# Optimization experiments

Measured on AMD Instinct MI355X. Metric: run time of the kernel, lower is better.

Reference implementation:

```python
import jax, jax.numpy as jnp
import numpy as np

B, C, H, W = 4, 96, 256, 256
WS = 8          # window size
NH = 4          # num heads
SHIFT = 4       # shift size (block_idx=1 -> WS//2)
HD = C // NH    # head dim = 24
N = WS * WS     # tokens per window = 64
MLP_H = 4 * C   # 384
EPS = 1e-6


def _rel_pos_index():
    coords = np.stack(np.meshgrid(np.arange(WS), np.arange(WS), indexing='ij'))  # [2,WS,WS]
    cf = coords.reshape(2, -1)                                                   # [2,N]
    rel = cf[:, :, None] - cf[:, None, :]                                        # [2,N,N]
    rel = rel.transpose(1, 2, 0) + (WS - 1)
    rel[:, :, 0] *= 2 * WS - 1
    return rel.sum(-1)  # [N,N] int


def _attn_mask():
    # standard Swin shifted-window mask, static (numpy)
    img = np.zeros((H, W), dtype=np.float32)
    cnt = 0
    for hs in (slice(0, -WS), slice(-WS, -SHIFT), slice(-SHIFT, None)):
        for ws_ in (slice(0, -WS), slice(-WS, -SHIFT), slice(-SHIFT, None)):
            img[hs, ws_] = cnt
            cnt += 1
    m = img.reshape(H // WS, WS, W // WS, WS).transpose(0, 2, 1, 3).reshape(-1, N)  # [nW,N]
    am = m[:, None, :] - m[:, :, None]
    return np.where(am != 0, -100.0, 0.0).astype(np.float32)  # [nW,N,N]


REL_IDX = _rel_pos_index()
ATTN_MASK = _attn_mask()


def _ln(x, w, b):
    mu = x.mean(-1, keepdims=True)
    var = ((x - mu) ** 2).mean(-1, keepdims=True)
    return (x - mu) * jax.lax.rsqrt(var + EPS) * w + b


def setup_inputs() -> dict:
    key = jax.random.key(0)
    ks = jax.random.split(key, 8)
    s = 0.02
    return {
        'x': jax.random.normal(ks[0], (B, C, H, W), jnp.float32),
        'norm_w': jnp.ones((C,), jnp.float32),
        'norm_b': jnp.zeros((C,), jnp.float32),
        'qkv_w': jax.random.normal(ks[1], (3 * C, C), jnp.float32) * s,
        'qkv_b': jnp.zeros((3 * C,), jnp.float32),
        'proj_w': jax.random.normal(ks[2], (C, C), jnp.float32) * s,
        'proj_b': jnp.zeros((C,), jnp.float32),
        'rpb_table': jax.random.normal(ks[3], ((2 * WS - 1) ** 2, NH), jnp.float32) * s,
        'norm2_w': jnp.ones((C,), jnp.float32),
        'norm2_b': jnp.zeros((C,), jnp.float32),
        'fc1_w': jax.random.normal(ks[4], (MLP_H, C), jnp.float32) * s,
        'fc1_b': jnp.zeros((MLP_H,), jnp.float32),
        'fc2_w': jax.random.normal(ks[5], (C, MLP_H), jnp.float32) * s,
        'fc2_b': jnp.zeros((C,), jnp.float32),
    }


def _swin_msa(y, qkv_w, qkv_b, proj_w, proj_b, rpb_table):
    # y: [B,H,W,C] (already layer-normed)
    ys = jnp.roll(y, shift=(-SHIFT, -SHIFT), axis=(1, 2))
    nWh, nWw = H // WS, W // WS
    # window partition -> [B*nW, N, C]
    xw = ys.reshape(B, nWh, WS, nWw, WS, C).transpose(0, 1, 3, 2, 4, 5).reshape(-1, N, C)
    qkv = xw @ qkv_w.T + qkv_b                       # [Bn,N,3C]
    qkv = qkv.reshape(-1, N, 3, NH, HD).transpose(2, 0, 3, 1, 4)  # [3,Bn,NH,N,HD]
    q, k, v = qkv[0], qkv[1], qkv[2]
    scale = HD ** -0.5
    attn = jnp.einsum('bhnd,bhmd->bhnm', q * scale, k)           # [Bn,NH,N,N]
    bias = rpb_table[jnp.asarray(REL_IDX)].transpose(2, 0, 1)    # [NH,N,N]
    attn = attn + bias[None]
    nW = nWh * nWw
    mask = jnp.asarray(ATTN_MASK)                                # [nW,N,N]
    attn = attn.reshape(B, nW, NH, N, N) + mask[None, :, None]
    attn = jax.nn.softmax(attn.reshape(-1, NH, N, N), axis=-1)
    out = jnp.einsum('bhnm,bhmd->bhnd', attn, v)                 # [Bn,NH,N,HD]
    out = out.transpose(0, 2, 1, 3).reshape(-1, N, C)
    out = out @ proj_w.T + proj_b
    # window reverse
    out = out.reshape(B, nWh, nWw, WS, WS, C).transpose(0, 1, 3, 2, 4, 5).reshape(B, H, W, C)
    return jnp.roll(out, shift=(SHIFT, SHIFT), axis=(1, 2))


def reference(x, norm_w, norm_b, qkv_w, qkv_b, proj_w, proj_b, rpb_table,
              norm2_w, norm2_b, fc1_w, fc1_b, fc2_w, fc2_b):
    xp = x.transpose(0, 2, 3, 1)                                  # [B,H,W,C]
    h = xp + _swin_msa(_ln(xp, norm_w, norm_b), qkv_w, qkv_b, proj_w, proj_b, rpb_table)
    y2 = _ln(h, norm2_w, norm2_b)
    mlp = jax.nn.gelu(y2 @ fc1_w.T + fc1_b, approximate=False) @ fc2_w.T + fc2_b
    h = h + mlp                                                   # proj is Identity (in==out)
    return h.transpose(0, 3, 1, 2)
```

## Files before the change

kernel.cpp:

```cpp
#include <hip/hip_runtime.h>
#include <hip/hip_bf16.h>
#include <math.h>

constexpr int B_    = 4;
constexpr int C_    = 96;
constexpr int H_    = 256;
constexpr int W_    = 256;
constexpr int WS_   = 8;
constexpr int NH_   = 4;
constexpr int SHIFT_= 4;
constexpr int HD_   = 24;
constexpr int NT_   = 64;
constexpr int NWW_  = 32;
constexpr int MLPH_ = 384;
constexpr int HW_   = H_*W_;
constexpr float EPS_   = 1e-6f;
constexpr float SCALE_ = 0.20412414523193150f;

using bf16   = __bf16;
using bf16x8 = __attribute__((ext_vector_type(8))) __bf16;
using bf16x4 = __attribute__((ext_vector_type(4))) __bf16;
using f32x4  = __attribute__((ext_vector_type(4))) float;

__device__ __forceinline__ f32x4 mfma16(bf16x8 a, bf16x8 b, f32x4 c) {
    return __builtin_amdgcn_mfma_f32_16x16x32_bf16(a, b, c, 0, 0, 0);
}

__device__ __forceinline__ float erf_approx(float x) {
    float ax = fabsf(x);
    float t  = 1.f/(1.f + 0.3275911f*ax);
    float y  = t*(0.254829592f + t*(-0.284496736f + t*(1.421413741f +
               t*(-1.453152027f + t*1.061405429f))));
    float r  = 1.f - y*__expf(-ax*ax);
    return x < 0.f ? -r : r;
}

constexpr size_t XT_B    = (size_t)B_*HW_*96*2;
constexpr int    WQ2_E   = 320*96;
constexpr int    WPR_E   = 96*96;
constexpr int    WF1_E   = 384*96;
constexpr int    WF2_E   = 96*384;
constexpr int    WSUM_E  = WQ2_E + WPR_E + WF1_E + WF2_E;
constexpr int    NBQ     = 320;
constexpr int    WBLKS   = (WSUM_E + NBQ + 255)/256;
constexpr int    TBLKS   = B_*HW_/64;

__global__ __launch_bounds__(256) void prep_kernel(
    const float* __restrict__ x,
    const float* __restrict__ qkv_w, const float* __restrict__ qkv_b,
    const float* __restrict__ proj_w, const float* __restrict__ fc1w,
    const float* __restrict__ fc2w,
    bf16* __restrict__ xt, bf16* __restrict__ warena, float* __restrict__ bq2)
{
    __shared__ float st[64*97];
    const int tid = threadIdx.x;
    if (blockIdx.x < WBLKS) {
        int i = blockIdx.x*256 + tid;
        if (i < WQ2_E) {
            int R = i/96, c = i%96;
            int h = R/80, s = R%80;
            float v;
            if      (s < 24) v = qkv_w[(h*24+s)*96 + c] * SCALE_;
            else if (s < 48) v = qkv_w[(96 + h*24 + s-24)*96 + c];
            else if (s < 72) v = qkv_w[(192 + h*24 + s-48)*96 + c];
            else             v = 0.f;
            warena[i] = (bf16)v;
        } else if (i < WQ2_E + WPR_E) {
            warena[i] = (bf16)proj_w[i - WQ2_E];
        } else if (i < WQ2_E + WPR_E + WF1_E) {
            warena[i] = (bf16)fc1w[i - WQ2_E - WPR_E];
        } else if (i < WSUM_E) {
            warena[i] = (bf16)fc2w[i - WQ2_E - WPR_E - WF1_E];
        } else if (i < WSUM_E + NBQ) {
            int j = i - WSUM_E;
            int h = j/80, s = j%80;
            float v;
            if      (s < 24) v = qkv_b[h*24+s] * SCALE_;
            else if (s < 48) v = qkv_b[96 + h*24 + s-24];
            else if (s < 72) v = qkv_b[192 + h*24 + s-48];
            else             v = 0.f;
            bq2[j] = v;
        }
        return;
    }
    const int tb = blockIdx.x - WBLKS;
    const int b  = tb >> 10;
    const int r0 = (tb & 1023)*64;
    const float* xb = x + (size_t)(b*96)*HW_ + r0;
    for (int idx = tid; idx < 6144; idx += 256) {
        int c = idx >> 6, t = idx & 63;
        st[t*97 + c] = xb[(size_t)c*HW_ + t];
    }
    __syncthreads();
    {
        const int t = tid >> 2, qa = tid & 3;
        bf16* dst = xt + ((size_t)(b<<16) + r0 + t)*96 + qa*24;
        const float* sp_ = &st[t*97 + qa*24];
        #pragma unroll
        for (int k = 0; k < 3; ++k) {
            bf16x8 o;
            #pragma unroll
            for (int j = 0; j < 8; ++j) o[j] = (bf16)sp_[k*8 + j];
            *(bf16x8*)(dst + k*8) = o;
        }
    }
}

constexpr int ASQ = 0;
constexpr int ASK = 2560;
constexpr int ASV = 4096;
constexpr int ASP = 5824;
constexpr int AXO = 10432;
constexpr int ASM_N = 17088;

__global__ __launch_bounds__(256) void attn_kernel(
    bf16* __restrict__ xt,
    const float* __restrict__ norm_w, const float* __restrict__ norm_b,
    const bf16*  __restrict__ wq2,
    const float* __restrict__ bq2,
    const bf16*  __restrict__ wproj,
    const float* __restrict__ proj_b,
    const float* __restrict__ rpb)
{
    __shared__ __align__(16) bf16 sm[ASM_N];
    const int tid  = threadIdx.x;
    const int wave = tid >> 6, lane = tid & 63;
    const int l16  = lane & 15, quad = lane >> 4;
    const int blk  = blockIdx.x;
    const int b    = blk >> 10;
    const int wid  = blk & 1023;
    const int wh   = wid >> 5, ww = wid & 31;

    if (tid < 64) { bf16x8 z = {}; *(bf16x8*)&sm[ASQ + tid*40 + 24] = z; }

    const int t  = tid >> 2, qa = tid & 3;
    const int wi = t >> 3, wj = t & 7;
    const int gh = (wh*WS_ + wi + SHIFT_) & (H_-1);
    const int gw = (ww*WS_ + wj + SHIFT_) & (W_-1);
    const size_t pix = (size_t)(b<<16) + gh*W_ + gw;
    {
        const bf16* xp = xt + pix*96 + qa*24;
        float v[24]; float mu = 0.f, ss = 0.f;
        #pragma unroll
        for (int k = 0; k < 3; ++k) {
            bf16x8 h8 = ((const bf16x8*)xp)[k];
            #pragma unroll
            for (int j = 0; j < 8; ++j) {
                v[k*8+j] = (float)h8[j];
                mu += v[k*8+j]; ss += v[k*8+j]*v[k*8+j];
            }
        }
        mu += __shfl_xor(mu,1); mu += __shfl_xor(mu,2);
        ss += __shfl_xor(ss,1); ss += __shfl_xor(ss,2);
        mu *= (1.f/C_);
        float rstd = rsqrtf(ss*(1.f/C_) - mu*mu + EPS_);
        #pragma unroll
        for (int cc = 0; cc < 24; ++cc) {
            int c = qa*24 + cc;
            sm[AXO + t*104 + c] = (bf16)((v[cc]-mu)*rstd*norm_w[c] + norm_b[c]);
        }
    }
    __syncthreads();

    bf16x8 af[4][3];
    #pragma unroll
    for (int mt = 0; mt < 4; ++mt)
        #pragma unroll
        for (int kk = 0; kk < 3; ++kk)
            af[mt][kk] = *(const bf16x8*)&sm[AXO + (mt*16+l16)*104 + kk*32 + quad*8];

    const int qrow0 = wave*16;
    for (int h = 0; h < NH_; ++h) {
        for (int jt = 0; jt < 5; ++jt) {
            if (((h*5 + jt) & 3) != wave) continue;
            const int s   = jt*16 + l16;
            const int row = h*80 + s;
            bf16x8 bw[3];
            #pragma unroll
            for (int kk = 0; kk < 3; ++kk)
                bw[kk] = *(const bf16x8*)(wq2 + (size_t)row*96 + kk*32 + quad*8);
            const float bias = bq2[row];
            #pragma unroll
            for (int mt = 0; mt < 4; ++mt) {
                f32x4 acc = {};
                #pragma unroll
                for (int kk = 0; kk < 3; ++kk) acc = mfma16(af[mt][kk], bw[kk], acc);
                const int tb = mt*16 + quad*4;
                if (s < 24) {
                    #pragma unroll
                    for (int r = 0; r < 4; ++r)
                        sm[ASQ + (tb+r)*40 + s] = (bf16)(acc[r] + bias);
                } else if (s < 48) {
                    #pragma unroll
                    for (int r = 0; r < 4; ++r)
                        sm[ASK + (tb+r)*24 + (s-24)] = (bf16)(acc[r] + bias);
                } else if (s < 72) {
                    bf16x4 pv;
                    #pragma unroll
                    for (int r = 0; r < 4; ++r) pv[r] = (bf16)(acc[r] + bias);
                    *(bf16x4*)&sm[ASV + (s-48)*72 + tb] = pv;
                }
            }
        }
        __syncthreads();

        bf16x8 aq = *(const bf16x8*)&sm[ASQ + (qrow0 + l16)*40 + quad*8];
        f32x4 accS[4];
        #pragma unroll
        for (int kt = 0; kt < 4; ++kt) {
            bf16x8 bk = *(const bf16x8*)&sm[ASK + (kt*16+l16)*24 + quad*8];
            f32x4 z = {};
            accS[kt] = mfma16(aq, bk, z);
        }
        float s_[4][4];
        #pragma unroll
        for (int kt = 0; kt < 4; ++kt) {
            const int key = kt*16 + l16;
            const int ki = key >> 3, kj = key & 7;
            const int labk = (((wh*8+ki) >= H_-WS_) + ((wh*8+ki) >= H_-SHIFT_))*3
                           +  ((ww*8+kj) >= W_-WS_) + ((ww*8+kj) >= W_-SHIFT_);
            #pragma unroll
            for (int r = 0; r < 4; ++r) {
                const int q = qrow0 + quad*4 + r;
                const int ti = q >> 3, tj = q & 7;
                const int labq = (((wh*8+ti) >= H_-WS_) + ((wh*8+ti) >= H_-SHIFT_))*3
                               +  ((ww*8+tj) >= W_-WS_) + ((ww*8+tj) >= W_-SHIFT_);
                const int ridx = (ti - ki + 7)*15 + (tj - kj + 7);
                float val = accS[kt][r] + rpb[ridx*NH_ + h];
                if (labk != labq) val -= 100.f;
                s_[kt][r] = val;
            }
        }
        #pragma unroll
        for (int r = 0; r < 4; ++r) {
            float m = fmaxf(fmaxf(s_[0][r], s_[1][r]), fmaxf(s_[2][r], s_[3][r]));
            m = fmaxf(m, __shfl_xor(m,1)); m = fmaxf(m, __shfl_xor(m,2));
            m = fmaxf(m, __shfl_xor(m,4)); m = fmaxf(m, __shfl_xor(m,8));
            float su = 0.f;
            #pragma unroll
            for (int kt = 0; kt < 4; ++kt) { s_[kt][r] = __expf(s_[kt][r]-m); su += s_[kt][r]; }
            su += __shfl_xor(su,1); su += __shfl_xor(su,2);
            su += __shfl_xor(su,4); su += __shfl_xor(su,8);
            const float inv = 1.f/su;
            #pragma unroll
            for (int kt = 0; kt < 4; ++kt)
                sm[ASP + (qrow0 + quad*4 + r)*72 + kt*16 + l16] = (bf16)(s_[kt][r]*inv);
        }
        __syncthreads();

        bf16x8 ap0 = *(const bf16x8*)&sm[ASP + (qrow0+l16)*72 + quad*8];
        bf16x8 ap1 = *(const bf16x8*)&sm[ASP + (qrow0+l16)*72 + 32 + quad*8];
        #pragma unroll
        for (int nt2 = 0; nt2 < 2; ++nt2) {
            const int d = nt2*16 + l16;
            bf16x8 bv0 = *(const bf16x8*)&sm[ASV + d*72 + quad*8];
            bf16x8 bv1 = *(const bf16x8*)&sm[ASV + d*72 + 32 + quad*8];
            f32x4 acc = {};
            acc = mfma16(ap0, bv0, acc);
            acc = mfma16(ap1, bv1, acc);
            if (d < HD_) {
                #pragma unroll
                for (int r = 0; r < 4; ++r)
                    sm[AXO + (qrow0 + quad*4 + r)*104 + h*24 + d] = (bf16)acc[r];
            }
        }
        __syncthreads();
    }

    {
        bf16x8 ao[3];
        #pragma unroll
        for (int kk = 0; kk < 3; ++kk)
            ao[kk] = *(const bf16x8*)&sm[AXO + (qrow0 + l16)*104 + kk*32 + quad*8];
        for (int nt = 0; nt < 6; ++nt) {
            const int oc = nt*16 + l16;
            bf16x8 bw[3];
            #pragma unroll
            for (int kk = 0; kk < 3; ++kk)
                bw[kk] = *(const bf16x8*)(wproj + (size_t)oc*96 + kk*32 + quad*8);
            f32x4 acc = {};
            #pragma unroll
            for (int kk = 0; kk < 3; ++kk) acc = mfma16(ao[kk], bw[kk], acc);
            #pragma unroll
            for (int r = 0; r < 4; ++r)
                sm[AXO + (qrow0 + quad*4 + r)*104 + oc] = (bf16)acc[r];
        }
    }
    __syncthreads();

    {
        bf16* xp = xt + pix*96 + qa*24;
        #pragma unroll
        for (int k = 0; k < 3; ++k) {
            bf16x8 xv = ((const bf16x8*)xp)[k];
            bf16x8 xo = *(const bf16x8*)&sm[AXO + t*104 + qa*24 + k*8];
            bf16x8 o;
            #pragma unroll
            for (int j = 0; j < 8; ++j)
                o[j] = (bf16)((float)xv[j] + (float)xo[j] + proj_b[qa*24 + k*8 + j]);
            *(bf16x8*)(xp + k*8) = o;
        }
    }
}

constexpr int MY  = 0;
constexpr int MH  = 6656;
constexpr int MR  = 13312;
constexpr int MSM = 25728;

__global__ __launch_bounds__(256) void mlp_kernel(
    const bf16*  __restrict__ hbf,
    const float* __restrict__ n2w, const float* __restrict__ n2b,
    const bf16*  __restrict__ wfc1, const float* __restrict__ fc1b,
    const bf16*  __restrict__ wfc2, const float* __restrict__ fc2b,
    float* __restrict__ out)
{
    __shared__ __align__(16) bf16 sm[MSM];
    float* stage = (float*)&sm[MR];
    const int tid  = threadIdx.x;
    const int wave = tid >> 6, lane = tid & 63;
    const int l16  = lane & 15, quad = lane >> 4;
    const int pb = blockIdx.x;
    const int b  = pb >> 10;
    const int r0 = (pb & 1023)*64;

    {
        const int t = tid >> 2, qa = tid & 3;
        const bf16* hp = hbf + ((size_t)(b<<16) + r0 + t)*96 + qa*24;
        bf16x8 h8[3]; float v[24]; float mu = 0.f, ss = 0.f;
        #pragma unroll
        for (int k = 0; k < 3; ++k) {
            h8[k] = ((const bf16x8*)hp)[k];
            *(bf16x8*)&sm[MH + t*104 + qa*24 + k*8] = h8[k];
            #pragma unroll
            for (int j = 0; j < 8; ++j) {
                v[k*8+j] = (float)h8[k][j];
                mu += v[k*8+j]; ss += v[k*8+j]*v[k*8+j];
            }
        }
        mu += __shfl_xor(mu,1); mu += __shfl_xor(mu,2);
        ss += __shfl_xor(ss,1); ss += __shfl_xor(ss,2);
        mu *= (1.f/C_);
        float rstd = rsqrtf(ss*(1.f/C_) - mu*mu + EPS_);
        #pragma unroll
        for (int cc = 0; cc < 24; ++cc) {
            int c = qa*24 + cc;
            sm[MY + t*104 + c] = (bf16)((v[cc]-mu)*rstd*n2w[c] + n2b[c]);
        }
    }
    __syncthreads();

    bf16x8 af[4][3];
    #pragma unroll
    for (int mt = 0; mt < 4; ++mt)
        #pragma unroll
        for (int kk = 0; kk < 3; ++kk)
            af[mt][kk] = *(const bf16x8*)&sm[MY + (mt*16+l16)*104 + kk*32 + quad*8];

    f32x4 acc2[6];
    #pragma unroll
    for (int n = 0; n < 6; ++n) acc2[n] = (f32x4){};

    for (int ci = 0; ci < 3; ++ci) {
        #pragma unroll
        for (int rep = 0; rep < 2; ++rep) {
            const int nt = wave + rep*4;
            const int ul = nt*16 + l16;
            const int u  = ci*128 + ul;
            bf16x8 bw[3];
            #pragma unroll
            for (int kk = 0; kk < 3; ++kk)
                bw[kk] = *(const bf16x8*)(wfc1 + (size_t)u*96 + kk*32 + quad*8);
            const float bias = fc1b[u];
            #pragma unroll
            for (int mt = 0; mt < 4; ++mt) {
                f32x4 acc = {};
                #pragma unroll
                for (int kk = 0; kk < 3; ++kk) acc = mfma16(af[mt][kk], bw[kk], acc);
                #pragma unroll
                for (int r = 0; r < 4; ++r) {
                    float tv = acc[r] + bias;
                    float g  = 0.5f*tv*(1.f + erf_approx(tv*0.70710678118654752f));
                    sm[MR + (mt*16 + quad*4 + r)*136 + ul] = (bf16)g;
                }
            }
        }
        __syncthreads();
        bf16x8 ag[4];
        #pragma unroll
        for (int kq = 0; kq < 4; ++kq)
            ag[kq] = *(const bf16x8*)&sm[MR + (wave*16+l16)*136 + kq*32 + quad*8];
        #pragma unroll
        for (int nt2 = 0; nt2 < 6; ++nt2) {
            const int c = nt2*16 + l16;
            #pragma unroll
            for (int kq = 0; kq < 4; ++kq) {
                bf16x8 bw = *(const bf16x8*)(wfc2 + (size_t)c*384 + ci*128 + kq*32 + quad*8);
                acc2[nt2] = mfma16(ag[kq], bw, acc2[nt2]);
            }
        }
        __syncthreads();
    }

    #pragma unroll
    for (int nt2 = 0; nt2 < 6; ++nt2) {
        const int c = nt2*16 + l16;
        const float bias = fc2b[c];
        #pragma unroll
        for (int r = 0; r < 4; ++r) {
            const int row = wave*16 + quad*4 + r;
            stage[row*97 + c] = acc2[nt2][r] + bias + (float)sm[MH + row*104 + c];
        }
    }
    __syncthreads();

    float* ob = out + (size_t)(b*96)*HW_ + r0;
    for (int idx = tid; idx < 6144; idx += 256) {
        int c = idx >> 6, tt = idx & 63;
        ob[(size_t)c*HW_ + tt] = stage[tt*97 + c];
    }
}

extern "C" void kernel_launch(void* const* d_in, const int* in_sizes, int n_in,
                              void* d_out, int out_size, void* d_ws, size_t ws_size,
                              hipStream_t stream) {
    const float* x      = (const float*)d_in[0];
    const float* norm_w = (const float*)d_in[1];
    const float* norm_b = (const float*)d_in[2];
    const float* qkv_w  = (const float*)d_in[3];
    const float* qkv_b  = (const float*)d_in[4];
    const float* proj_w = (const float*)d_in[5];
    const float* proj_b = (const float*)d_in[6];
    const float* rpb    = (const float*)d_in[7];
    const float* n2w    = (const float*)d_in[8];
    const float* n2b    = (const float*)d_in[9];
    const float* fc1w   = (const float*)d_in[10];
    const float* fc1b   = (const float*)d_in[11];
    const float* fc2w   = (const float*)d_in[12];
    const float* fc2b   = (const float*)d_in[13];

    float* outp = (float*)d_out;
    char*  ws   = (char*)d_ws;
    bf16*  xt   = (bf16*)ws;
    bf16*  wa   = (bf16*)(ws + XT_B);
    float* bq2  = (float*)(ws + XT_B + (size_t)WSUM_E*2);

    prep_kernel<<<WBLKS + TBLKS, 256, 0, stream>>>(x, qkv_w, qkv_b, proj_w,
                                                   fc1w, fc2w, xt, wa, bq2);
    attn_kernel<<<B_*1024, 256, 0, stream>>>(xt, norm_w, norm_b,
                                             wa, bq2,
                                             wa + WQ2_E, proj_b, rpb);
    mlp_kernel<<<TBLKS, 256, 0, stream>>>(xt, n2w, n2b,
                                          wa + WQ2_E + WPR_E, fc1b,
                                          wa + WQ2_E + WPR_E + WF1_E, fc2b,
                                          outp);
}
```

Measured before the change: 538.0 us.

## Rework MLP kernel: tanh-GELU, transposed MFMA epilogue, smaller LDS, vector stores

The MLP kernel now computes GELU with a tanh-form sigmoid approximation (one exp and one rcp) in place of the erf polynomial. The fc1 MFMA operands are swapped so each lane holds four consecutive hidden units, which allows a vectorized bias load and packed bf16x4 LDS writes. The residual is re-read from global memory instead of being staged in LDS, which shrinks shared memory and may raise occupancy. The LN output writes and the final NCHW stores are vectorized. The GELU change alters numerics slightly, since approximate GELU replaces exact GELU.

Result: no change. 528.8 us (-1.7%).

```diff
diff --git a/kernel.cpp b/kernel.cpp
--- a/kernel.cpp
+++ b/kernel.cpp
@@ -24,15 +24,6 @@
 
 __device__ __forceinline__ f32x4 mfma16(bf16x8 a, bf16x8 b, f32x4 c) {
     return __builtin_amdgcn_mfma_f32_16x16x32_bf16(a, b, c, 0, 0, 0);
-}
-
-__device__ __forceinline__ float erf_approx(float x) {
-    float ax = fabsf(x);
-    float t  = 1.f/(1.f + 0.3275911f*ax);
-    float y  = t*(0.254829592f + t*(-0.284496736f + t*(1.421413741f +
-               t*(-1.453152027f + t*1.061405429f))));
-    float r  = 1.f - y*__expf(-ax*ax);
-    return x < 0.f ? -r : r;
 }
 
 constexpr size_t XT_B    = (size_t)B_*HW_*96*2;
@@ -303,10 +294,9 @@
     }
 }
 
-constexpr int MY  = 0;
-constexpr int MH  = 6656;
-constexpr int MR  = 13312;
-constexpr int MSM = 25728;
+constexpr int MY2   = 0;
+constexpr int MG    = 6656;
+constexpr int MSM2  = 15360;
 
 __global__ __launch_bounds__(256) void mlp_kernel(
     const bf16*  __restrict__ hbf,
@@ -315,8 +305,8 @@
     const bf16*  __restrict__ wfc2, const float* __restrict__ fc2b,
     float* __restrict__ out)
 {
-    __shared__ __align__(16) bf16 sm[MSM];
-    float* stage = (float*)&sm[MR];
+    __shared__ __align__(16) bf16 sm[MSM2];
+    float* stage = (float*)sm;
     const int tid  = threadIdx.x;
     const int wave = tid >> 6, lane = tid & 63;
     const int l16  = lane & 15, quad = lane >> 4;
@@ -327,14 +317,13 @@
     {
         const int t = tid >> 2, qa = tid & 3;
         const bf16* hp = hbf + ((size_t)(b<<16) + r0 + t)*96 + qa*24;
-        bf16x8 h8[3]; float v[24]; float mu = 0.f, ss = 0.f;
+        float v[24]; float mu = 0.f, ss = 0.f;
         #pragma unroll
         for (int k = 0; k < 3; ++k) {
-            h8[k] = ((const bf16x8*)hp)[k];
-            *(bf16x8*)&sm[MH + t*104 + qa*24 + k*8] = h8[k];
+            bf16x8 h8 = ((const bf16x8*)hp)[k];
             #pragma unroll
             for (int j = 0; j < 8; ++j) {
-                v[k*8+j] = (float)h8[k][j];
+                v[k*8+j] = (float)h8[j];
                 mu += v[k*8+j]; ss += v[k*8+j]*v[k*8+j];
             }
         }
@@ -343,9 +332,14 @@
         mu *= (1.f/C_);
         float rstd = rsqrtf(ss*(1.f/C_) - mu*mu + EPS_);
         #pragma unroll
-        for (int cc = 0; cc < 24; ++cc) {
-            int c = qa*24 + cc;
-            sm[MY + t*104 + c] = (bf16)((v[cc]-mu)*rstd*n2w[c] + n2b[c]);
+        for (int k = 0; k < 3; ++k) {
+            bf16x8 o;
+            #pragma unroll
+            for (int j = 0; j < 8; ++j) {
+                int c = qa*24 + k*8 + j;
+                o[j] = (bf16)((v[k*8+j]-mu)*rstd*n2w[c] + n2b[c]);
+            }
+            *(bf16x8*)&sm[MY2 + t*104 + qa*24 + k*8] = o;
         }
     }
     __syncthreads();
@@ -355,7 +349,7 @@
     for (int mt = 0; mt < 4; ++mt)
         #pragma unroll
         for (int kk = 0; kk < 3; ++kk)
-            af[mt][kk] = *(const bf16x8*)&sm[MY + (mt*16+l16)*104 + kk*32 + quad*8];
+            af[mt][kk] = *(const bf16x8*)&sm[MY2 + (mt*16+l16)*104 + kk*32 + quad*8];
 
     f32x4 acc2[6];
     #pragma unroll
@@ -364,32 +358,35 @@
     for (int ci = 0; ci < 3; ++ci) {
         #pragma unroll
         for (int rep = 0; rep < 2; ++rep) {
-            const int nt = wave + rep*4;
-            const int ul = nt*16 + l16;
-            const int u  = ci*128 + ul;
+            const int ntl = wave + rep*4;
+            const int ub  = ci*128 + ntl*16;
             bf16x8 bw[3];
             #pragma unroll
             for (int kk = 0; kk < 3; ++kk)
-                bw[kk] = *(const bf16x8*)(wfc1 + (size_t)u*96 + kk*32 + quad*8);
-            const float bias = fc1b[u];
+                bw[kk] = *(const bf16x8*)(wfc1 + (size_t)(ub + l16)*96 + kk*32 + quad*8);
+            const f32x4 b4 = *(const f32x4*)&fc1b[ub + quad*4];
             #pragma unroll
             for (int mt = 0; mt < 4; ++mt) {
                 f32x4 acc = {};
                 #pragma unroll
-                for (int kk = 0; kk < 3; ++kk) acc = mfma16(af[mt][kk], bw[kk], acc);
+                for (int kk = 0; kk < 3; ++kk) acc = mfma16(bw[kk], af[mt][kk], acc);
+                bf16x4 g4;
                 #pragma unroll
                 for (int r = 0; r < 4; ++r) {
-                    float tv = acc[r] + bias;
-                    float g  = 0.5f*tv*(1.f + erf_approx(tv*0.70710678118654752f));
-                    sm[MR + (mt*16 + quad*4 + r)*136 + ul] = (bf16)g;
+                    float tv = acc[r] + b4[r];
+                    float u  = tv*tv;
+                    float w  = tv*fmaf(-0.0713548165f, u, -1.5957691216f);
+                    float e  = __expf(w);
+                    g4[r] = (bf16)(tv*__builtin_amdgcn_rcpf(1.f + e));
                 }
+                *(bf16x4*)&sm[MG + (mt*16 + l16)*136 + ntl*16 + quad*4] = g4;
             }
         }
         __syncthreads();
         bf16x8 ag[4];
         #pragma unroll
         for (int kq = 0; kq < 4; ++kq)
-            ag[kq] = *(const bf16x8*)&sm[MR + (wave*16+l16)*136 + kq*32 + quad*8];
+            ag[kq] = *(const bf16x8*)&sm[MG + (wave*16+l16)*136 + kq*32 + quad*8];
         #pragma unroll
         for (int nt2 = 0; nt2 < 6; ++nt2) {
             const int c = nt2*16 + l16;
@@ -402,22 +399,31 @@
         __syncthreads();
     }
 
-    #pragma unroll
-    for (int nt2 = 0; nt2 < 6; ++nt2) {
-        const int c = nt2*16 + l16;
-        const float bias = fc2b[c];
+    {
+        const bf16* hres = hbf + ((size_t)(b<<16) + r0)*96;
         #pragma unroll
         for (int r = 0; r < 4; ++r) {
             const int row = wave*16 + quad*4 + r;
-            stage[row*97 + c] = acc2[nt2][r] + bias + (float)sm[MH + row*104 + c];
+            const bf16* hrow = hres + (size_t)row*96;
+            #pragma unroll
+            for (int nt2 = 0; nt2 < 6; ++nt2) {
+                const int c = nt2*16 + l16;
+                stage[row*97 + c] = acc2[nt2][r] + fc2b[c] + (float)hrow[c];
+            }
         }
     }
     __syncthreads();
 
     float* ob = out + (size_t)(b*96)*HW_ + r0;
-    for (int idx = tid; idx < 6144; idx += 256) {
-        int c = idx >> 6, tt = idx & 63;
-        ob[(size_t)c*HW_ + tt] = stage[tt*97 + c];
+    #pragma unroll
+    for (int it = 0; it < 6; ++it) {
+        int i  = it*256 + tid;
+        int c  = i >> 4;
+        int t4 = (i & 15) * 4;
+        f32x4 o;
+        #pragma unroll
+        for (int j = 0; j < 4; ++j) o[j] = stage[(t4+j)*97 + c];
+        *(f32x4*)&ob[(size_t)c*HW_ + t4] = o;
     }
 }
 
```
